# Performance work log

Hardware: AMD Instinct MI355X
Metric: run time of the kernel (lower is better)

## Reference

```python
import jax, jax.numpy as jnp
import numpy as np

# attn_reps = "8x0n+30x1n": per head channel C = 8 scalars + 30 Lorentz four-vectors (4 each) = 128
N_SCALARS, N_VECTORS = 8, 30
ETA = jnp.diag(jnp.array([1.0, -1.0, -1.0, -1.0], dtype=jnp.float32))  # Minkowski metric


def _quat_to_rot(q):
    # q: (M,4) unit quaternions -> (M,3,3) rotation matrices
    w, x, y, z = q[:, 0], q[:, 1], q[:, 2], q[:, 3]
    r0 = jnp.stack([1 - 2 * (y * y + z * z), 2 * (x * y - w * z), 2 * (x * z + w * y)], axis=-1)
    r1 = jnp.stack([2 * (x * y + w * z), 1 - 2 * (x * x + z * z), 2 * (y * z - w * x)], axis=-1)
    r2 = jnp.stack([2 * (x * z - w * y), 2 * (y * z + w * x), 1 - 2 * (x * x + y * y)], axis=-1)
    return jnp.stack([r0, r1, r2], axis=-2)


def _random_lorentz(key, M):
    # random proper Lorentz transforms: boost(beta) @ blockdiag(1, R)
    k1, k2 = jax.random.split(key)
    quat = jax.random.normal(k1, (M, 4), dtype=jnp.float32)
    quat = quat / jnp.linalg.norm(quat, axis=-1, keepdims=True)
    R = _quat_to_rot(quat)  # (M,3,3)
    beta = jax.random.uniform(k2, (M, 3), minval=-1.0, maxval=1.0, dtype=jnp.float32) * (0.6 / np.sqrt(3.0))
    b2 = jnp.sum(beta * beta, axis=-1)  # (M,), < 0.36
    gamma = 1.0 / jnp.sqrt(1.0 - b2)
    n = beta / jnp.sqrt(jnp.maximum(b2, 1e-12))[:, None]
    gb = gamma[:, None] * beta  # (M,3)
    top = jnp.concatenate([gamma[:, None], gb], axis=-1)[:, None, :]  # (M,1,4)
    spatial = jnp.eye(3, dtype=jnp.float32) + (gamma - 1.0)[:, None, None] * n[:, :, None] * n[:, None, :]
    bottom = jnp.concatenate([gb[:, :, None], spatial], axis=-1)  # (M,3,4)
    B = jnp.concatenate([top, bottom], axis=-2)  # (M,4,4) boost
    rot4 = jnp.zeros((M, 4, 4), dtype=jnp.float32).at[:, 0, 0].set(1.0).at[:, 1:, 1:].set(R)
    return jnp.einsum('mij,mjk->mik', B, rot4)


def setup_inputs() -> dict:
    key = jax.random.key(0)
    kq, kk, kv, kl = jax.random.split(key, 4)
    B, H, N, C = 8, 8, 1024, 128
    q = jax.random.normal(kq, (B, H, N, C), dtype=jnp.float32)
    k = jax.random.normal(kk, (B, H, N, C), dtype=jnp.float32)
    v = jax.random.normal(kv, (B, H, N, C), dtype=jnp.float32)
    L = _random_lorentz(kl, B * N).reshape(B, N, 4, 4)
    return {"q_local": q, "k_local": k, "v_local": v, "lframes_matrices": L}


def _transform(x, M):
    # TensorRepsTransform: scalars pass through, four-vectors get v' = M v (per particle)
    # x: (B,H,N,C), M: (B,N,4,4)
    s = x[..., :N_SCALARS]
    vec = x[..., N_SCALARS:].reshape(x.shape[:-1] + (N_VECTORS, 4))
    vec = jnp.einsum('bnij,bhnvj->bhnvi', M, vec)
    return jnp.concatenate([s, vec.reshape(x.shape[:-1] + (N_VECTORS * 4,))], axis=-1)


def reference(q_local, k_local, v_local, lframes_matrices):
    C = q_local.shape[-1]
    # InverseLFrames: Lorentz inverse  Lambda^{-1} = eta Lambda^T eta
    inv = jnp.einsum('ij,bnkj,kl->bnil', ETA, lframes_matrices, ETA)
    # LowerIndices: lower the output index -> eta @ Lambda^{-1}
    lower_inv = jnp.einsum('ij,bnjk->bnik', ETA, inv)
    q_g = _transform(q_local, inv)
    k_g = _transform(k_local, lower_inv)
    v_g = _transform(v_local, inv)
    # standard SDPA (scale 1/sqrt(C))
    scores = jnp.einsum('bhqc,bhkc->bhqk', q_g, k_g) * (1.0 / np.sqrt(C))
    attn = jax.nn.softmax(scores, axis=-1)
    out_g = jnp.einsum('bhqk,bhkc->bhqc', attn, v_g)
    # back to local frame with Lambda itself
    return _transform(out_g, lframes_matrices)
```

## Files before the change

kernel.cpp:

```cpp
#include <hip/hip_runtime.h>
#include <math.h>

typedef _Float16 f16;
typedef _Float16 f16x2 __attribute__((ext_vector_type(2)));
typedef _Float16 f16x4 __attribute__((ext_vector_type(4)));
typedef _Float16 f16x8 __attribute__((ext_vector_type(8)));
typedef float    f32x4 __attribute__((ext_vector_type(4)));
typedef float    f32x16 __attribute__((ext_vector_type(16)));

typedef const __attribute__((address_space(1))) void gv_t;
typedef __attribute__((address_space(3))) void lv_t;

#define NSEQ 1024
#define CD   128
#define LT   136


__global__ __launch_bounds__(256)
void ipa_pre(const float* __restrict__ kg, const float* __restrict__ vg,
             const float* __restrict__ Lm, f16* __restrict__ khs, f16* __restrict__ vhs)
{
    __shared__ float LL[64 * 16];
    __shared__ __align__(16) f16 Kt[64 * LT];
    __shared__ __align__(16) f16 Vt[64 * LT];
    const int bx = blockIdx.x, nt = blockIdx.y, tid = threadIdx.x;
    const int bh = ((bx & 7) << 3) | (bx >> 3);
    const int b  = bh >> 3;
    const float* Lb = Lm + ((size_t)b * NSEQ + nt * 64) * 16;
    for (int t = tid; t < 64 * 16; t += 256) LL[t] = Lb[t];
    __syncthreads();

    const size_t base = ((size_t)bh * NSEQ + nt * 64) * CD;
    #pragma unroll
    for (int it = 0; it < 8; ++it) {
        int g = it * 256 + tid;
        int row = g >> 5, cg = g & 31;
        size_t idx = base + row * CD + cg * 4;
        const float* Lr = &LL[row * 16];
        float4 xk = *(const float4*)(kg + idx);
        float4 xv = *(const float4*)(vg + idx);
        float4 yk = xk, yv = xv;
        if (cg >= 2) {
            float t0 = xk.x, t1 = -xk.y, t2 = -xk.z, t3 = -xk.w;
            yk.x = Lr[0]*t0 + Lr[4]*t1 + Lr[8] *t2 + Lr[12]*t3;
            yk.y = Lr[1]*t0 + Lr[5]*t1 + Lr[9] *t2 + Lr[13]*t3;
            yk.z = Lr[2]*t0 + Lr[6]*t1 + Lr[10]*t2 + Lr[14]*t3;
            yk.w = Lr[3]*t0 + Lr[7]*t1 + Lr[11]*t2 + Lr[15]*t3;
            t0 = xv.x; t1 = -xv.y; t2 = -xv.z; t3 = -xv.w;
            yv.x =  (Lr[0]*t0 + Lr[4]*t1 + Lr[8] *t2 + Lr[12]*t3);
            yv.y = -(Lr[1]*t0 + Lr[5]*t1 + Lr[9] *t2 + Lr[13]*t3);
            yv.z = -(Lr[2]*t0 + Lr[6]*t1 + Lr[10]*t2 + Lr[14]*t3);
            yv.w = -(Lr[3]*t0 + Lr[7]*t1 + Lr[11]*t2 + Lr[15]*t3);
        }
        f16x4 hk = {(f16)yk.x, (f16)yk.y, (f16)yk.z, (f16)yk.w};
        f16x4 hv = {(f16)yv.x, (f16)yv.y, (f16)yv.z, (f16)yv.w};
        *(f16x4*)&Kt[row * LT + cg * 4] = hk;
        *(f16x4*)&Vt[row * LT + cg * 4] = hv;
    }
    __syncthreads();

    f16* kout = khs + (size_t)bh * 131072 + (size_t)(nt * 2) * 4096;
    #pragma unroll
    for (int it = 0; it < 4; ++it) {
        int slot = it * 256 + tid;
        int kt2 = slot >> 9, cs16 = (slot >> 6) & 7, L = slot & 63;
        int lq5 = L & 31, h = L >> 5;
        f16x8 kv = *(const f16x8*)&Kt[(kt2 * 32 + lq5) * LT + cs16 * 16 + 8 * h];
        *(f16x8*)(kout + (size_t)kt2 * 4096 + cs16 * 512 + L * 8) = kv;
    }
    f16* vout = vhs + (size_t)bh * 131072 + (size_t)(nt * 2) * 4096;
    #pragma unroll
    for (int it = 0; it < 4; ++it) {
        int slot = it * 256 + tid;
        int kt2 = slot >> 9, cb = (slot >> 7) & 3, kh = (slot >> 6) & 1, L = slot & 63;
        int lq5 = L & 31, h = L >> 5;
        int c = cb * 32 + lq5;
        f16x8 o;
        #pragma unroll
        for (int j = 0; j < 8; ++j)
            o[j] = Vt[(kt2 * 32 + kh * 16 + 8 * h + j) * LT + c];
        *(f16x8*)(vout + (size_t)kt2 * 4096 + (cb * 2 + kh) * 512 + L * 8) = o;
    }
}

static __device__ __forceinline__ unsigned pk2(f16 a, f16 b) {
    union { f16x2 h; unsigned u; } x; x.h = (f16x2){a, b}; return x.u;
}

__global__ __launch_bounds__(256, 2)
void ipa_attn(const float* __restrict__ qg, const f16* __restrict__ khs,
              const f16* __restrict__ vhs, const float* __restrict__ Lm,
              float* __restrict__ out)
{
    __shared__ __align__(16) f16 sK[2][4096];
    __shared__ __align__(16) f16 sV[2][4096];
    const int n = blockIdx.x;
    const int bh = ((n & 7) << 3) | ((n >> 3) & 7);
    const int b  = bh >> 3;
    const int tid = threadIdx.x;
    const int w = tid >> 6, lane = tid & 63;
    const int lq5 = lane & 31, hh = lane >> 5;
    const int qblk = n >> 6;
    const int q0 = qblk * 128 + w * 32;
    const f16* kbh = khs + (size_t)bh * 131072;
    const f16* vbh = vhs + (size_t)bh * 131072;
    const float sc2 = 0.12751744154226873f;

    auto stage = [&](int nb, int it) {
        const char* kp = (const char*)(kbh + (size_t)it * 4096);
        const char* vp = (const char*)(vbh + (size_t)it * 4096);
        char* kd = (char*)&sK[nb][0];
        char* vd = (char*)&sV[nb][0];
        #pragma unroll
        for (int j = 0; j < 2; ++j) {
            int off = (w * 2 + j) * 1024;
            __builtin_amdgcn_global_load_lds((gv_t*)(kp + off + lane * 16),
                                             (lv_t*)(kd + off), 16, 0, 0);
            __builtin_amdgcn_global_load_lds((gv_t*)(vp + off + lane * 16),
                                             (lv_t*)(vd + off), 16, 0, 0);
        }
    };

    f16x8 qf[8];
    {
        int qrow = q0 + lq5;
        const float* Lr = Lm + ((size_t)b * NSEQ + qrow) * 16;
        const float* qp = qg + ((size_t)bh * NSEQ + qrow) * CD;
        float Lv[16];
        #pragma unroll
        for (int i = 0; i < 4; ++i) *(float4*)&Lv[i*4] = *(const float4*)(Lr + i*4);
        #pragma unroll
        for (int cs = 0; cs < 8; ++cs) {
            int c0 = cs * 16 + 8 * hh;
            float4 x0 = *(const float4*)(qp + c0);
            float4 x1 = *(const float4*)(qp + c0 + 4);
            if (c0 >= 8) {
                float t0 = x0.x, t1 = -x0.y, t2 = -x0.z, t3 = -x0.w;
                float4 y;
                y.x =  (Lv[0]*t0 + Lv[4]*t1 + Lv[8] *t2 + Lv[12]*t3);
                y.y = -(Lv[1]*t0 + Lv[5]*t1 + Lv[9] *t2 + Lv[13]*t3);
                y.z = -(Lv[2]*t0 + Lv[6]*t1 + Lv[10]*t2 + Lv[14]*t3);
                y.w = -(Lv[3]*t0 + Lv[7]*t1 + Lv[11]*t2 + Lv[15]*t3);
                x0 = y;
                t0 = x1.x; t1 = -x1.y; t2 = -x1.z; t3 = -x1.w;
                y.x =  (Lv[0]*t0 + Lv[4]*t1 + Lv[8] *t2 + Lv[12]*t3);
                y.y = -(Lv[1]*t0 + Lv[5]*t1 + Lv[9] *t2 + Lv[13]*t3);
                y.z = -(Lv[2]*t0 + Lv[6]*t1 + Lv[10]*t2 + Lv[14]*t3);
                y.w = -(Lv[3]*t0 + Lv[7]*t1 + Lv[11]*t2 + Lv[15]*t3);
                x1 = y;
            }
            qf[cs] = (f16x8){(f16)(x0.x*sc2), (f16)(x0.y*sc2), (f16)(x0.z*sc2), (f16)(x0.w*sc2),
                             (f16)(x1.x*sc2), (f16)(x1.y*sc2), (f16)(x1.z*sc2), (f16)(x1.w*sc2)};
        }
    }

    f32x16 oacc[4];
    #pragma unroll
    for (int cb = 0; cb < 4; ++cb)
        #pragma unroll
        for (int r = 0; r < 16; ++r) oacc[cb][r] = 0.f;
    float mrun = -1e30f, lrun = 0.f;

    stage(0, 0);

    for (int it = 0; it < 32; ++it) {
        const int cur = it & 1;
        __syncthreads();
        if (it < 31) stage(cur ^ 1, it + 1);

        const f16* kb = &sK[cur][0];
        const f16* vb = &sV[cur][0];

        f32x16 s;
        #pragma unroll
        for (int r = 0; r < 16; ++r) s[r] = 0.f;
        #pragma unroll
        for (int cs = 0; cs < 8; ++cs) {
            f16x8 kf = *(const f16x8*)&kb[cs * 512 + lane * 8];
            s = __builtin_amdgcn_mfma_f32_32x32x16_f16(kf, qf[cs], s, 0, 0, 0);
        }

        float mx = fmaxf(s[0], s[1]);
        #pragma unroll
        for (int r = 2; r < 16; ++r) mx = fmaxf(mx, s[r]);
        mx = fmaxf(mx, __shfl_xor(mx, 32, 64));
        float mnew = fmaxf(mrun, mx);
        if (!__all(mx <= mrun)) {
            float alpha = exp2f(mrun - mnew);
            lrun *= alpha;
            #pragma unroll
            for (int cb = 0; cb < 4; ++cb) oacc[cb] *= alpha;
            mrun = mnew;
        }
        float pr[16];
        f16 ph[16];
        #pragma unroll
        for (int r = 0; r < 16; ++r) { pr[r] = exp2f(s[r] - mnew); ph[r] = (f16)pr[r]; }
        float rs = ((pr[0]+pr[1])+(pr[2]+pr[3])) + ((pr[4]+pr[5])+(pr[6]+pr[7]))
                 + ((pr[8]+pr[9])+(pr[10]+pr[11])) + ((pr[12]+pr[13])+(pr[14]+pr[15]));
        lrun += rs;

        f16x8 pf[2];
        #pragma unroll
        for (int kh = 0; kh < 2; ++kh) {
            unsigned wA0 = pk2(ph[8*kh+0], ph[8*kh+1]);
            unsigned wA1 = pk2(ph[8*kh+2], ph[8*kh+3]);
            unsigned wB0 = pk2(ph[8*kh+4], ph[8*kh+5]);
            unsigned wB1 = pk2(ph[8*kh+6], ph[8*kh+7]);
            unsigned send0 = hh ? wA0 : wB0;
            unsigned send1 = hh ? wA1 : wB1;
            unsigned recv0 = __shfl_xor(send0, 32, 64);
            unsigned recv1 = __shfl_xor(send1, 32, 64);
            union { unsigned u[4]; f16x8 h; } pw;
            pw.u[0] = hh ? recv0 : wA0;
            pw.u[1] = hh ? recv1 : wA1;
            pw.u[2] = hh ? wB0 : recv0;
            pw.u[3] = hh ? wB1 : recv1;
            pf[kh] = pw.h;
        }

        #pragma unroll
        for (int cb = 0; cb < 4; ++cb)
            #pragma unroll
            for (int kh = 0; kh < 2; ++kh) {
                f16x8 vf = *(const f16x8*)&vb[(cb * 2 + kh) * 512 + lane * 8];
                oacc[cb] = __builtin_amdgcn_mfma_f32_32x32x16_f16(vf, pf[kh], oacc[cb], 0, 0, 0);
            }
    }

    {
        float l = lrun + __shfl_xor(lrun, 32, 64);
        float invl = 1.0f / l;
        int qrow = q0 + lq5;
        const float* Lr = Lm + ((size_t)b * NSEQ + qrow) * 16;
        float Lv[16];
        #pragma unroll
        for (int i = 0; i < 4; ++i) *(float4*)&Lv[i*4] = *(const float4*)(Lr + i*4);
        float* ob = out + ((size_t)bh * NSEQ + qrow) * CD;
        #pragma unroll
        for (int cb = 0; cb < 4; ++cb) {
            #pragma unroll
            for (int rg = 0; rg < 4; ++rg) {
                int c0 = cb * 32 + rg * 8 + 4 * hh;
                float o0 = oacc[cb][rg*4+0] * invl, o1 = oacc[cb][rg*4+1] * invl;
                float o2 = oacc[cb][rg*4+2] * invl, o3 = oacc[cb][rg*4+3] * invl;
                float4 r;
                if (c0 >= 8) {
                    r.x = Lv[0] *o0 + Lv[1] *o1 + Lv[2] *o2 + Lv[3] *o3;
                    r.y = Lv[4] *o0 + Lv[5] *o1 + Lv[6] *o2 + Lv[7] *o3;
                    r.z = Lv[8] *o0 + Lv[9] *o1 + Lv[10]*o2 + Lv[11]*o3;
                    r.w = Lv[12]*o0 + Lv[13]*o1 + Lv[14]*o2 + Lv[15]*o3;
                } else {
                    r.x = o0; r.y = o1; r.z = o2; r.w = o3;
                }
                *(float4*)(ob + c0) = r;
            }
        }
    }
}

extern "C" void kernel_launch(void* const* d_in, const int* in_sizes, int n_in,
                              void* d_out, int out_size, void* d_ws, size_t ws_size,
                              hipStream_t stream) {
    const float* q = (const float*)d_in[0];
    const float* k = (const float*)d_in[1];
    const float* v = (const float*)d_in[2];
    const float* L = (const float*)d_in[3];
    float* o = (float*)d_out;
    f16* khs = (f16*)d_ws;
    f16* vhs = khs + (size_t)64 * 131072;
    dim3 grid1(64, 16);
    ipa_pre<<<grid1, 256, 0, stream>>>(k, v, L, khs, vhs);
    ipa_attn<<<512, 256, 0, stream>>>(q, khs, vhs, L, o);
}
```

Baseline: 197.6 us.

## Load K/V fragments directly from global memory and process two key tiles per iteration

Drops the LDS double-buffered staging of K/V (global_load_lds plus __syncthreads) and has each wave read its pre-swizzled f16 K/V fragments straight from global memory, relying on L2/cache reuse across the 4 waves. The loop now handles two 32-key tiles per step, sharing one online-softmax max/rescale across both. It also removes the min-occupancy-2 launch bound. This removes the barrier and LDS traffic but adds redundant global reads per wave and higher register pressure, which may cost occupancy or add exposed load latency.

```diff
diff --git a/kernel.cpp b/kernel.cpp
--- a/kernel.cpp
+++ b/kernel.cpp
@@ -7,9 +7,6 @@
 typedef _Float16 f16x8 __attribute__((ext_vector_type(8)));
 typedef float    f32x4 __attribute__((ext_vector_type(4)));
 typedef float    f32x16 __attribute__((ext_vector_type(16)));
-
-typedef const __attribute__((address_space(1))) void gv_t;
-typedef __attribute__((address_space(3))) void lv_t;
 
 #define NSEQ 1024
 #define CD   128
@@ -87,13 +84,11 @@
     union { f16x2 h; unsigned u; } x; x.h = (f16x2){a, b}; return x.u;
 }
 
-__global__ __launch_bounds__(256, 2)
+__global__ __launch_bounds__(256)
 void ipa_attn(const float* __restrict__ qg, const f16* __restrict__ khs,
               const f16* __restrict__ vhs, const float* __restrict__ Lm,
               float* __restrict__ out)
 {
-    __shared__ __align__(16) f16 sK[2][4096];
-    __shared__ __align__(16) f16 sV[2][4096];
     const int n = blockIdx.x;
     const int bh = ((n & 7) << 3) | ((n >> 3) & 7);
     const int b  = bh >> 3;
@@ -105,21 +100,6 @@
     const f16* kbh = khs + (size_t)bh * 131072;
     const f16* vbh = vhs + (size_t)bh * 131072;
     const float sc2 = 0.12751744154226873f;
-
-    auto stage = [&](int nb, int it) {
-        const char* kp = (const char*)(kbh + (size_t)it * 4096);
-        const char* vp = (const char*)(vbh + (size_t)it * 4096);
-        char* kd = (char*)&sK[nb][0];
-        char* vd = (char*)&sV[nb][0];
-        #pragma unroll
-        for (int j = 0; j < 2; ++j) {
-            int off = (w * 2 + j) * 1024;
-            __builtin_amdgcn_global_load_lds((gv_t*)(kp + off + lane * 16),
-                                             (lv_t*)(kd + off), 16, 0, 0);
-            __builtin_amdgcn_global_load_lds((gv_t*)(vp + off + lane * 16),
-                                             (lv_t*)(vd + off), 16, 0, 0);
-        }
-    };
 
     f16x8 qf[8];
     {
@@ -161,28 +141,23 @@
         for (int r = 0; r < 16; ++r) oacc[cb][r] = 0.f;
     float mrun = -1e30f, lrun = 0.f;
 
-    stage(0, 0);
-
-    for (int it = 0; it < 32; ++it) {
-        const int cur = it & 1;
-        __syncthreads();
-        if (it < 31) stage(cur ^ 1, it + 1);
-
-        const f16* kb = &sK[cur][0];
-        const f16* vb = &sV[cur][0];
-
-        f32x16 s;
-        #pragma unroll
-        for (int r = 0; r < 16; ++r) s[r] = 0.f;
+    for (int t16 = 0; t16 < 16; ++t16) {
+        const int tA = t16 * 2, tB = tA + 1;
+
+        f32x16 sA, sB;
+        #pragma unroll
+        for (int r = 0; r < 16; ++r) { sA[r] = 0.f; sB[r] = 0.f; }
         #pragma unroll
         for (int cs = 0; cs < 8; ++cs) {
-            f16x8 kf = *(const f16x8*)&kb[cs * 512 + lane * 8];
-            s = __builtin_amdgcn_mfma_f32_32x32x16_f16(kf, qf[cs], s, 0, 0, 0);
-        }
-
-        float mx = fmaxf(s[0], s[1]);
-        #pragma unroll
-        for (int r = 2; r < 16; ++r) mx = fmaxf(mx, s[r]);
+            f16x8 kfA = *(const f16x8*)(kbh + ((size_t)tA * 8 + cs) * 512 + lane * 8);
+            f16x8 kfB = *(const f16x8*)(kbh + ((size_t)tB * 8 + cs) * 512 + lane * 8);
+            sA = __builtin_amdgcn_mfma_f32_32x32x16_f16(kfA, qf[cs], sA, 0, 0, 0);
+            sB = __builtin_amdgcn_mfma_f32_32x32x16_f16(kfB, qf[cs], sB, 0, 0, 0);
+        }
+
+        float mx = fmaxf(sA[0], sB[0]);
+        #pragma unroll
+        for (int r = 1; r < 16; ++r) mx = fmaxf(mx, fmaxf(sA[r], sB[r]));
         mx = fmaxf(mx, __shfl_xor(mx, 32, 64));
         float mnew = fmaxf(mrun, mx);
         if (!__all(mx <= mrun)) {
@@ -192,40 +167,65 @@
             for (int cb = 0; cb < 4; ++cb) oacc[cb] *= alpha;
             mrun = mnew;
         }
-        float pr[16];
-        f16 ph[16];
-        #pragma unroll
-        for (int r = 0; r < 16; ++r) { pr[r] = exp2f(s[r] - mnew); ph[r] = (f16)pr[r]; }
-        float rs = ((pr[0]+pr[1])+(pr[2]+pr[3])) + ((pr[4]+pr[5])+(pr[6]+pr[7]))
-                 + ((pr[8]+pr[9])+(pr[10]+pr[11])) + ((pr[12]+pr[13])+(pr[14]+pr[15]));
+        float prA[16], prB[16];
+        f16 phA[16], phB[16];
+        #pragma unroll
+        for (int r = 0; r < 16; ++r) {
+            prA[r] = exp2f(sA[r] - mnew); phA[r] = (f16)prA[r];
+            prB[r] = exp2f(sB[r] - mnew); phB[r] = (f16)prB[r];
+        }
+        float rs = 0.f;
+        #pragma unroll
+        for (int r = 0; r < 16; ++r) rs += prA[r] + prB[r];
         lrun += rs;
 
-        f16x8 pf[2];
+        f16x8 pfA[2], pfB[2];
         #pragma unroll
         for (int kh = 0; kh < 2; ++kh) {
-            unsigned wA0 = pk2(ph[8*kh+0], ph[8*kh+1]);
-            unsigned wA1 = pk2(ph[8*kh+2], ph[8*kh+3]);
-            unsigned wB0 = pk2(ph[8*kh+4], ph[8*kh+5]);
-            unsigned wB1 = pk2(ph[8*kh+6], ph[8*kh+7]);
-            unsigned send0 = hh ? wA0 : wB0;
-            unsigned send1 = hh ? wA1 : wB1;
-            unsigned recv0 = __shfl_xor(send0, 32, 64);
-            unsigned recv1 = __shfl_xor(send1, 32, 64);
+            unsigned aA0 = pk2(phA[8*kh+0], phA[8*kh+1]);
+            unsigned aA1 = pk2(phA[8*kh+2], phA[8*kh+3]);
+            unsigned aB0 = pk2(phA[8*kh+4], phA[8*kh+5]);
+            unsigned aB1 = pk2(phA[8*kh+6], phA[8*kh+7]);
+            unsigned s0 = hh ? aA0 : aB0;
+            unsigned s1 = hh ? aA1 : aB1;
+            unsigned r0 = __shfl_xor(s0, 32, 64);
+            unsigned r1 = __shfl_xor(s1, 32, 64);
             union { unsigned u[4]; f16x8 h; } pw;
-            pw.u[0] = hh ? recv0 : wA0;
-            pw.u[1] = hh ? recv1 : wA1;
-            pw.u[2] = hh ? wB0 : recv0;
-            pw.u[3] = hh ? wB1 : recv1;
-            pf[kh] = pw.h;
-        }
-
-        #pragma unroll
-        for (int cb = 0; cb < 4; ++cb)
+            pw.u[0] = hh ? r0 : aA0;
+            pw.u[1] = hh ? r1 : aA1;
+            pw.u[2] = hh ? aB0 : r0;
+            pw.u[3] = hh ? aB1 : r1;
+            pfA[kh] = pw.h;
+
+            unsigned bA0 = pk2(phB[8*kh+0], phB[8*kh+1]);
+            unsigned bA1 = pk2(phB[8*kh+2], phB[8*kh+3]);
+            unsigned bB0 = pk2(phB[8*kh+4], phB[8*kh+5]);
+            unsigned bB1 = pk2(phB[8*kh+6], phB[8*kh+7]);
+            unsigned t0 = hh ? bA0 : bB0;
+            unsigned t1 = hh ? bA1 : bB1;
+            unsigned u0 = __shfl_xor(t0, 32, 64);
+            unsigned u1 = __shfl_xor(t1, 32, 64);
+            union { unsigned u[4]; f16x8 h; } qw;
+            qw.u[0] = hh ? u0 : bA0;
+            qw.u[1] = hh ? u1 : bA1;
+            qw.u[2] = hh ? bB0 : u0;
+            qw.u[3] = hh ? bB1 : u1;
+            pfB[kh] = qw.h;
+        }
+
+        #pragma unroll
+        for (int cb = 0; cb < 4; ++cb) {
             #pragma unroll
             for (int kh = 0; kh < 2; ++kh) {
-                f16x8 vf = *(const f16x8*)&vb[(cb * 2 + kh) * 512 + lane * 8];
-                oacc[cb] = __builtin_amdgcn_mfma_f32_32x32x16_f16(vf, pf[kh], oacc[cb], 0, 0, 0);
-            }
+                f16x8 vfA = *(const f16x8*)(vbh + ((size_t)tA * 8 + cb * 2 + kh) * 512 + lane * 8);
+                oacc[cb] = __builtin_amdgcn_mfma_f32_32x32x16_f16(vfA, pfA[kh], oacc[cb], 0, 0, 0);
+            }
+            #pragma unroll
+            for (int kh = 0; kh < 2; ++kh) {
+                f16x8 vfB = *(const f16x8*)(vbh + ((size_t)tB * 8 + cb * 2 + kh) * 512 + lane * 8);
+                oacc[cb] = __builtin_amdgcn_mfma_f32_32x32x16_f16(vfB, pfB[kh], oacc[cb], 0, 0, 0);
+            }
+        }
     }
 
     {
```

After: 210.4 us. 6.5% more time.

## Fuse K/V Lorentz preprocessing into attention kernel with register-prefetch pipeline

Applied to the files above, without the earlier changes.

Removes the separate preprocessing kernel that wrote fp16 K/V to workspace. Each attention block now loads fp32 K, V and frame matrices directly, transforms them in registers and writes them into padded, XOR-swizzled LDS tiles, with next-tile loads overlapped with the current MFMA work. MFMA sections are raised in priority with s_setprio. This drops a kernel launch and the workspace round trip. In exchange, every query block (8 per bh) redoes the K/V transform and reads twice the bytes in fp32, and the launch-bounds occupancy hint is dropped.

```diff
diff --git a/kernel.cpp b/kernel.cpp
--- a/kernel.cpp
+++ b/kernel.cpp
@@ -3,97 +3,21 @@
 
 typedef _Float16 f16;
 typedef _Float16 f16x2 __attribute__((ext_vector_type(2)));
-typedef _Float16 f16x4 __attribute__((ext_vector_type(4)));
 typedef _Float16 f16x8 __attribute__((ext_vector_type(8)));
-typedef float    f32x4 __attribute__((ext_vector_type(4)));
 typedef float    f32x16 __attribute__((ext_vector_type(16)));
-
-typedef const __attribute__((address_space(1))) void gv_t;
-typedef __attribute__((address_space(3))) void lv_t;
 
 #define NSEQ 1024
 #define CD   128
-#define LT   136
-
+#define KSTR 136
+#define VSTR 40
 
 __global__ __launch_bounds__(256)
-void ipa_pre(const float* __restrict__ kg, const float* __restrict__ vg,
-             const float* __restrict__ Lm, f16* __restrict__ khs, f16* __restrict__ vhs)
+void ipa_fused(const float* __restrict__ qg, const float* __restrict__ kg,
+               const float* __restrict__ vg, const float* __restrict__ Lm,
+               float* __restrict__ out)
 {
-    __shared__ float LL[64 * 16];
-    __shared__ __align__(16) f16 Kt[64 * LT];
-    __shared__ __align__(16) f16 Vt[64 * LT];
-    const int bx = blockIdx.x, nt = blockIdx.y, tid = threadIdx.x;
-    const int bh = ((bx & 7) << 3) | (bx >> 3);
-    const int b  = bh >> 3;
-    const float* Lb = Lm + ((size_t)b * NSEQ + nt * 64) * 16;
-    for (int t = tid; t < 64 * 16; t += 256) LL[t] = Lb[t];
-    __syncthreads();
-
-    const size_t base = ((size_t)bh * NSEQ + nt * 64) * CD;
-    #pragma unroll
-    for (int it = 0; it < 8; ++it) {
-        int g = it * 256 + tid;
-        int row = g >> 5, cg = g & 31;
-        size_t idx = base + row * CD + cg * 4;
-        const float* Lr = &LL[row * 16];
-        float4 xk = *(const float4*)(kg + idx);
-        float4 xv = *(const float4*)(vg + idx);
-        float4 yk = xk, yv = xv;
-        if (cg >= 2) {
-            float t0 = xk.x, t1 = -xk.y, t2 = -xk.z, t3 = -xk.w;
-            yk.x = Lr[0]*t0 + Lr[4]*t1 + Lr[8] *t2 + Lr[12]*t3;
-            yk.y = Lr[1]*t0 + Lr[5]*t1 + Lr[9] *t2 + Lr[13]*t3;
-            yk.z = Lr[2]*t0 + Lr[6]*t1 + Lr[10]*t2 + Lr[14]*t3;
-            yk.w = Lr[3]*t0 + Lr[7]*t1 + Lr[11]*t2 + Lr[15]*t3;
-            t0 = xv.x; t1 = -xv.y; t2 = -xv.z; t3 = -xv.w;
-            yv.x =  (Lr[0]*t0 + Lr[4]*t1 + Lr[8] *t2 + Lr[12]*t3);
-            yv.y = -(Lr[1]*t0 + Lr[5]*t1 + Lr[9] *t2 + Lr[13]*t3);
-            yv.z = -(Lr[2]*t0 + Lr[6]*t1 + Lr[10]*t2 + Lr[14]*t3);
-            yv.w = -(Lr[3]*t0 + Lr[7]*t1 + Lr[11]*t2 + Lr[15]*t3);
-        }
-        f16x4 hk = {(f16)yk.x, (f16)yk.y, (f16)yk.z, (f16)yk.w};
-        f16x4 hv = {(f16)yv.x, (f16)yv.y, (f16)yv.z, (f16)yv.w};
-        *(f16x4*)&Kt[row * LT + cg * 4] = hk;
-        *(f16x4*)&Vt[row * LT + cg * 4] = hv;
-    }
-    __syncthreads();
-
-    f16* kout = khs + (size_t)bh * 131072 + (size_t)(nt * 2) * 4096;
-    #pragma unroll
-    for (int it = 0; it < 4; ++it) {
-        int slot = it * 256 + tid;
-        int kt2 = slot >> 9, cs16 = (slot >> 6) & 7, L = slot & 63;
-        int lq5 = L & 31, h = L >> 5;
-        f16x8 kv = *(const f16x8*)&Kt[(kt2 * 32 + lq5) * LT + cs16 * 16 + 8 * h];
-        *(f16x8*)(kout + (size_t)kt2 * 4096 + cs16 * 512 + L * 8) = kv;
-    }
-    f16* vout = vhs + (size_t)bh * 131072 + (size_t)(nt * 2) * 4096;
-    #pragma unroll
-    for (int it = 0; it < 4; ++it) {
-        int slot = it * 256 + tid;
-        int kt2 = slot >> 9, cb = (slot >> 7) & 3, kh = (slot >> 6) & 1, L = slot & 63;
-        int lq5 = L & 31, h = L >> 5;
-        int c = cb * 32 + lq5;
-        f16x8 o;
-        #pragma unroll
-        for (int j = 0; j < 8; ++j)
-            o[j] = Vt[(kt2 * 32 + kh * 16 + 8 * h + j) * LT + c];
-        *(f16x8*)(vout + (size_t)kt2 * 4096 + (cb * 2 + kh) * 512 + L * 8) = o;
-    }
-}
-
-static __device__ __forceinline__ unsigned pk2(f16 a, f16 b) {
-    union { f16x2 h; unsigned u; } x; x.h = (f16x2){a, b}; return x.u;
-}
-
-__global__ __launch_bounds__(256, 2)
-void ipa_attn(const float* __restrict__ qg, const f16* __restrict__ khs,
-              const f16* __restrict__ vhs, const float* __restrict__ Lm,
-              float* __restrict__ out)
-{
-    __shared__ __align__(16) f16 sK[2][4096];
-    __shared__ __align__(16) f16 sV[2][4096];
+    __shared__ __align__(16) f16 Kt[2][32 * KSTR];
+    __shared__ __align__(16) f16 Vt[2][128 * VSTR];
     const int n = blockIdx.x;
     const int bh = ((n & 7) << 3) | ((n >> 3) & 7);
     const int b  = bh >> 3;
@@ -102,22 +26,70 @@
     const int lq5 = lane & 31, hh = lane >> 5;
     const int qblk = n >> 6;
     const int q0 = qblk * 128 + w * 32;
-    const f16* kbh = khs + (size_t)bh * 131072;
-    const f16* vbh = vhs + (size_t)bh * 131072;
     const float sc2 = 0.12751744154226873f;
 
-    auto stage = [&](int nb, int it) {
-        const char* kp = (const char*)(kbh + (size_t)it * 4096);
-        const char* vp = (const char*)(vbh + (size_t)it * 4096);
-        char* kd = (char*)&sK[nb][0];
-        char* vd = (char*)&sV[nb][0];
-        #pragma unroll
-        for (int j = 0; j < 2; ++j) {
-            int off = (w * 2 + j) * 1024;
-            __builtin_amdgcn_global_load_lds((gv_t*)(kp + off + lane * 16),
-                                             (lv_t*)(kd + off), 16, 0, 0);
-            __builtin_amdgcn_global_load_lds((gv_t*)(vp + off + lane * 16),
-                                             (lv_t*)(vd + off), 16, 0, 0);
+    const int krow = tid >> 3;
+    const int ce   = tid & 7;
+    const int vrot = (ce & 3) << 3;
+    const float* kgb = kg + ((size_t)bh * NSEQ) * CD + ce * 16;
+    const float* vgb = vg + ((size_t)bh * NSEQ) * CD + ce * 16;
+    const float* Lmb = Lm + ((size_t)b * NSEQ) * 16;
+
+    float4 kx[4], vx[4], Lx[4];
+    auto load_k = [&](int t) {
+        const float* p = kgb + (size_t)(t * 32 + krow) * CD;
+        #pragma unroll
+        for (int j = 0; j < 4; ++j) kx[j] = *(const float4*)(p + j * 4);
+    };
+    auto load_v = [&](int t) {
+        const float* p = vgb + (size_t)(t * 32 + krow) * CD;
+        #pragma unroll
+        for (int j = 0; j < 4; ++j) vx[j] = *(const float4*)(p + j * 4);
+    };
+    auto load_L = [&](int t) {
+        const float* p = Lmb + (size_t)(t * 32 + krow) * 16;
+        #pragma unroll
+        for (int j = 0; j < 4; ++j) Lx[j] = *(const float4*)(p + j * 4);
+    };
+    auto xk_write = [&](int nb) {
+        const float* Lv = (const float*)&Lx[0];
+        f16 oh[16];
+        #pragma unroll
+        for (int qd = 0; qd < 4; ++qd) {
+            float4 x = kx[qd], y = x;
+            int c0 = ce * 16 + qd * 4;
+            if (c0 >= 8) {
+                float t0 = x.x, t1 = -x.y, t2 = -x.z, t3 = -x.w;
+                y.x = Lv[0]*t0 + Lv[4]*t1 + Lv[8] *t2 + Lv[12]*t3;
+                y.y = Lv[1]*t0 + Lv[5]*t1 + Lv[9] *t2 + Lv[13]*t3;
+                y.z = Lv[2]*t0 + Lv[6]*t1 + Lv[10]*t2 + Lv[14]*t3;
+                y.w = Lv[3]*t0 + Lv[7]*t1 + Lv[11]*t2 + Lv[15]*t3;
+            }
+            oh[qd*4+0] = (f16)y.x; oh[qd*4+1] = (f16)y.y;
+            oh[qd*4+2] = (f16)y.z; oh[qd*4+3] = (f16)y.w;
+        }
+        *(f16x8*)&Kt[nb][krow * KSTR + ce * 16]     = *(f16x8*)&oh[0];
+        *(f16x8*)&Kt[nb][krow * KSTR + ce * 16 + 8] = *(f16x8*)&oh[8];
+    };
+    auto xv_write = [&](int nb) {
+        const float* Lv = (const float*)&Lx[0];
+        f16* vt = &Vt[nb][0];
+        const int ki = krow ^ vrot;
+        #pragma unroll
+        for (int qd = 0; qd < 4; ++qd) {
+            float4 x = vx[qd], y = x;
+            int c0 = ce * 16 + qd * 4;
+            if (c0 >= 8) {
+                float t0 = x.x, t1 = -x.y, t2 = -x.z, t3 = -x.w;
+                y.x =  (Lv[0]*t0 + Lv[4]*t1 + Lv[8] *t2 + Lv[12]*t3);
+                y.y = -(Lv[1]*t0 + Lv[5]*t1 + Lv[9] *t2 + Lv[13]*t3);
+                y.z = -(Lv[2]*t0 + Lv[6]*t1 + Lv[10]*t2 + Lv[14]*t3);
+                y.w = -(Lv[3]*t0 + Lv[7]*t1 + Lv[11]*t2 + Lv[15]*t3);
+            }
+            vt[(c0+0)*VSTR + ki] = (f16)y.x;
+            vt[(c0+1)*VSTR + ki] = (f16)y.y;
+            vt[(c0+2)*VSTR + ki] = (f16)y.z;
+            vt[(c0+3)*VSTR + ki] = (f16)y.w;
         }
     };
 
@@ -161,24 +133,26 @@
         for (int r = 0; r < 16; ++r) oacc[cb][r] = 0.f;
     float mrun = -1e30f, lrun = 0.f;
 
-    stage(0, 0);
-
-    for (int it = 0; it < 32; ++it) {
-        const int cur = it & 1;
-        __syncthreads();
-        if (it < 31) stage(cur ^ 1, it + 1);
-
-        const f16* kb = &sK[cur][0];
-        const f16* vb = &sV[cur][0];
+    load_k(0); load_L(0); load_v(0);
+    xk_write(0); xv_write(0);
+    __syncthreads();
+
+    for (int t = 0; t < 32; ++t) {
+        const int cur = t & 1, nxt = cur ^ 1;
+        if (t < 31) { load_k(t + 1); load_L(t + 1); }
 
         f32x16 s;
         #pragma unroll
         for (int r = 0; r < 16; ++r) s[r] = 0.f;
+        __builtin_amdgcn_s_setprio(1);
         #pragma unroll
         for (int cs = 0; cs < 8; ++cs) {
-            f16x8 kf = *(const f16x8*)&kb[cs * 512 + lane * 8];
+            f16x8 kf = *(const f16x8*)&Kt[cur][lq5 * KSTR + cs * 16 + hh * 8];
             s = __builtin_amdgcn_mfma_f32_32x32x16_f16(kf, qf[cs], s, 0, 0, 0);
         }
+        __builtin_amdgcn_s_setprio(0);
+
+        if (t < 31) { xk_write(nxt); load_v(t + 1); }
 
         float mx = fmaxf(s[0], s[1]);
         #pragma unroll
@@ -196,17 +170,17 @@
         f16 ph[16];
         #pragma unroll
         for (int r = 0; r < 16; ++r) { pr[r] = exp2f(s[r] - mnew); ph[r] = (f16)pr[r]; }
-        float rs = ((pr[0]+pr[1])+(pr[2]+pr[3])) + ((pr[4]+pr[5])+(pr[6]+pr[7]))
-                 + ((pr[8]+pr[9])+(pr[10]+pr[11])) + ((pr[12]+pr[13])+(pr[14]+pr[15]));
-        lrun += rs;
+        lrun += ((pr[0]+pr[1])+(pr[2]+pr[3])) + ((pr[4]+pr[5])+(pr[6]+pr[7]))
+              + ((pr[8]+pr[9])+(pr[10]+pr[11])) + ((pr[12]+pr[13])+(pr[14]+pr[15]));
 
         f16x8 pf[2];
         #pragma unroll
         for (int kh = 0; kh < 2; ++kh) {
-            unsigned wA0 = pk2(ph[8*kh+0], ph[8*kh+1]);
-            unsigned wA1 = pk2(ph[8*kh+2], ph[8*kh+3]);
-            unsigned wB0 = pk2(ph[8*kh+4], ph[8*kh+5]);
-            unsigned wB1 = pk2(ph[8*kh+6], ph[8*kh+7]);
+            union { f16x2 h; unsigned u; } c0{{ph[8*kh+0], ph[8*kh+1]}},
+                                           c1{{ph[8*kh+2], ph[8*kh+3]}},
+                                           c2{{ph[8*kh+4], ph[8*kh+5]}},
+                                           c3{{ph[8*kh+6], ph[8*kh+7]}};
+            unsigned wA0 = c0.u, wA1 = c1.u, wB0 = c2.u, wB1 = c3.u;
             unsigned send0 = hh ? wA0 : wB0;
             unsigned send1 = hh ? wA1 : wB1;
             unsigned recv0 = __shfl_xor(send0, 32, 64);
@@ -219,13 +193,23 @@
             pf[kh] = pw.h;
         }
 
-        #pragma unroll
-        for (int cb = 0; cb < 4; ++cb)
+        __builtin_amdgcn_s_setprio(1);
+        #pragma unroll
+        for (int cb = 0; cb < 4; ++cb) {
+            const int c = cb * 32 + lq5;
+            const int rc = ((c >> 4) & 3) << 3;
             #pragma unroll
             for (int kh = 0; kh < 2; ++kh) {
-                f16x8 vf = *(const f16x8*)&vb[(cb * 2 + kh) * 512 + lane * 8];
+                f16x8 vf = *(const f16x8*)&Vt[cur][c * VSTR + ((kh * 16 + hh * 8) ^ rc)];
                 oacc[cb] = __builtin_amdgcn_mfma_f32_32x32x16_f16(vf, pf[kh], oacc[cb], 0, 0, 0);
             }
+        }
+        __builtin_amdgcn_s_setprio(0);
+
+        if (t < 31) {
+            xv_write(nxt);
+            __syncthreads();
+        }
     }
 
     {
@@ -267,9 +251,5 @@
     const float* v = (const float*)d_in[2];
     const float* L = (const float*)d_in[3];
     float* o = (float*)d_out;
-    f16* khs = (f16*)d_ws;
-    f16* vhs = khs + (size_t)64 * 131072;
-    dim3 grid1(64, 16);
-    ipa_pre<<<grid1, 256, 0, stream>>>(k, v, L, khs, vhs);
-    ipa_attn<<<512, 256, 0, stream>>>(q, khs, vhs, L, o);
+    ipa_fused<<<512, 256, 0, stream>>>(q, k, v, L, o);
 }
```

Measured after the change: 270.6 us. 1.37x slower.
